# Kernel optimization log

Measured on AMD Instinct MI355X. Metric: run time of the kernel, lower is better.

Reference implementation:

```python
import jax, jax.numpy as jnp
import numpy as np

DIM = 1024
HEADS = 8
DIM_HEAD = 64
INNER = HEADS * DIM_HEAD  # 512


def setup_inputs() -> dict:
    key = jax.random.key(0)
    k1, k2, k3, k4 = jax.random.split(key, 4)
    x = jax.random.normal(k1, (4, 4096, DIM), dtype=jnp.float32)
    # torch nn.Linear weights: [out_features, in_features]
    w_qkv = jax.random.normal(k2, (INNER * 3, DIM), dtype=jnp.float32) * (DIM ** -0.5)
    w_out = jax.random.normal(k3, (DIM, INNER), dtype=jnp.float32) * (INNER ** -0.5)
    b_out = jax.random.normal(k4, (DIM,), dtype=jnp.float32) * 0.01
    return {"x": x, "w_qkv": w_qkv, "w_out": w_out, "b_out": b_out}


def reference(x, w_qkv, w_out, b_out):
    b, n, _ = x.shape
    h, dh = HEADS, DIM_HEAD
    qkv = x @ w_qkv.T  # [b, n, 3*inner]
    q, k, v = jnp.split(qkv, 3, axis=-1)
    # [b, n, inner] -> [b, h, n, dh]
    reshape = lambda t: t.reshape(b, n, h, dh).transpose(0, 2, 1, 3)
    q, k, v = reshape(q), reshape(k), reshape(v)
    k = jax.nn.softmax(k, axis=-1)
    context = jnp.einsum('bhnd,bhne->bhde', k, v)   # [b, h, dh, dh]
    out = jnp.einsum('bhnd,bhde->bhne', q, context)  # [b, h, n, dh]
    out = out.transpose(0, 2, 1, 3).reshape(b, n, h * dh)
    return out @ w_out.T + b_out
```

## Files before the change

### kernel.cpp

```cpp
#include <hip/hip_runtime.h>
#include <hip/hip_bf16.h>

using bf16 = __hip_bfloat16;
typedef __attribute__((ext_vector_type(8))) short short8;
typedef __attribute__((ext_vector_type(4))) float floatx4;

#define NB 4
#define NSEQ 4096
#define DIM 1024
#define INNER 512
#define TOK (NB * NSEQ)


__device__ inline unsigned short f2bf(float x) {
  union { bf16 h; unsigned short u; } c; c.h = __float2bfloat16(x); return c.u;
}
__device__ inline float bf2f(unsigned short u) {
  return __uint_as_float((unsigned)u << 16);
}

__device__ inline void stage8(const bf16* __restrict__ src, bf16* dst) {
  *(uint4*)dst = *(const uint4*)src;
}
__device__ inline void stage8(const float* __restrict__ src, bf16* dst) {
  const float4 a = ((const float4*)src)[0];
  const float4 b = ((const float4*)src)[1];
  union { uint4 u; bf16 h[8]; } p;
  p.h[0] = __float2bfloat16(a.x); p.h[1] = __float2bfloat16(a.y);
  p.h[2] = __float2bfloat16(a.z); p.h[3] = __float2bfloat16(a.w);
  p.h[4] = __float2bfloat16(b.x); p.h[5] = __float2bfloat16(b.y);
  p.h[6] = __float2bfloat16(b.z); p.h[7] = __float2bfloat16(b.w);
  *(uint4*)dst = p.u;
}

__global__ __launch_bounds__(256)
void convert_x(const float* __restrict__ x, bf16* __restrict__ xb) {
  const size_t i = (size_t)blockIdx.x * 256 + threadIdx.x;
  stage8(x + i * 8, xb + i * 8);
}

__global__ __launch_bounds__(256)
void copy16(const uint4* __restrict__ src, uint4* __restrict__ dst) {
  const size_t i = (size_t)blockIdx.x * 256 + threadIdx.x;
  dst[i] = src[i];
}

__global__ void zero_ctx(float* __restrict__ ctx) {
  ((float4*)ctx)[blockIdx.x * 256 + threadIdx.x] = make_float4(0.f, 0.f, 0.f, 0.f);
}

template <typename TA, typename TW, typename TO, bool BIAS>
__global__ __launch_bounds__(256, 4)
void gemm_bt(const TA* __restrict__ A, int lda,
             const TW* __restrict__ W, size_t wbatch,
             const float* __restrict__ bias,
             TO* __restrict__ C, int ldc, int K) {
  __shared__ __align__(16) bf16 As[128 * 72];
  __shared__ __align__(16) bf16 Bs[128 * 72];

  const int tid  = threadIdx.x;
  const int m0   = blockIdx.y * 128;
  const int n0   = blockIdx.x * 128;
  if (wbatch) W += (size_t)(blockIdx.y >> 5) * wbatch;

  const int wave = tid >> 6;
  const int lane = tid & 63;
  const int wr   = (wave >> 1) * 64;
  const int wc   = (wave & 1) * 64;
  const int quad = lane >> 4;
  const int r16  = lane & 15;

  floatx4 acc[4][4];
#pragma unroll
  for (int i = 0; i < 4; ++i)
#pragma unroll
    for (int j = 0; j < 4; ++j) acc[i][j] = (floatx4)0.0f;

  const int ksteps = K >> 6;
  for (int kt = 0; kt < ksteps; ++kt) {
    const int k0 = kt << 6;
#pragma unroll
    for (int l = 0; l < 4; ++l) {
      const int s   = l * 256 + tid;
      const int row = s >> 3, sub = s & 7;
      stage8(A + (size_t)(m0 + row) * lda + k0 + sub * 8, As + row * 72 + sub * 8);
      stage8(W + (size_t)(n0 + row) * K   + k0 + sub * 8, Bs + row * 72 + sub * 8);
    }
    __syncthreads();
#pragma unroll
    for (int kk = 0; kk < 64; kk += 32) {
      short8 af[4], bfg[4];
#pragma unroll
      for (int i = 0; i < 4; ++i)
        af[i] = *(const short8*)(As + (wr + i * 16 + r16) * 72 + kk + quad * 8);
#pragma unroll
      for (int j = 0; j < 4; ++j)
        bfg[j] = *(const short8*)(Bs + (wc + j * 16 + r16) * 72 + kk + quad * 8);
#pragma unroll
      for (int i = 0; i < 4; ++i)
#pragma unroll
        for (int j = 0; j < 4; ++j)
          acc[i][j] = __builtin_amdgcn_mfma_f32_16x16x32_bf16(af[i], bfg[j], acc[i][j], 0, 0, 0);
    }
    __syncthreads();
  }

#pragma unroll
  for (int j = 0; j < 4; ++j) {
    const int col = n0 + wc + j * 16 + r16;
    const float bv = BIAS ? bias[col] : 0.0f;
#pragma unroll
    for (int i = 0; i < 4; ++i) {
      const int rowb = m0 + wr + i * 16 + quad * 4;
#pragma unroll
      for (int r = 0; r < 4; ++r) {
        const float v = acc[i][j][r] + bv;
        if constexpr (sizeof(TO) == 2)
          C[(size_t)(rowb + r) * ldc + col] = __float2bfloat16(v);
        else
          C[(size_t)(rowb + r) * ldc + col] = v;
      }
    }
  }
}

__global__ __launch_bounds__(256)
void softmax_context(const unsigned short* __restrict__ kv, float* __restrict__ ctx) {
  __shared__ unsigned short skT[64 * 130];
  __shared__ unsigned short vT [64 * 130];

  const int tid   = threadIdx.x;
  const int wave  = tid >> 6;
  const int lane  = tid & 63;
  const int bh    = blockIdx.x >> 4;
  const int slice = blockIdx.x & 15;
  const int b     = bh >> 3, h = bh & 7;

  const int quad = lane >> 4;
  const int r16  = lane & 15;
  const int d0   = wave * 16;

  floatx4 acc[4];
#pragma unroll
  for (int j = 0; j < 4; ++j) acc[j] = (floatx4)0.0f;

  const int rgrp = tid >> 3;
  const int c    = tid & 7;

  for (int ch = 0; ch < 2; ++ch) {
#pragma unroll
    for (int p = 0; p < 4; ++p) {
      const int r = p * 32 + rgrp;
      const size_t rowbase =
          (size_t)(b * NSEQ + slice * 256 + ch * 128 + r) * 1024 + h * 64;
      const uint4 k8 = *(const uint4*)(kv + rowbase + c * 8);
      const uint4 v8 = *(const uint4*)(kv + rowbase + 512 + c * 8);
      const unsigned short* kb = (const unsigned short*)&k8;
      const unsigned short* vb = (const unsigned short*)&v8;

      float kf[8];
#pragma unroll
      for (int j = 0; j < 8; ++j) kf[j] = bf2f(kb[j]);
      float mx = kf[0];
#pragma unroll
      for (int j = 1; j < 8; ++j) mx = fmaxf(mx, kf[j]);
      mx = fmaxf(mx, __shfl_xor(mx, 1, 64));
      mx = fmaxf(mx, __shfl_xor(mx, 2, 64));
      mx = fmaxf(mx, __shfl_xor(mx, 4, 64));
      float e[8]; float s = 0.0f;
#pragma unroll
      for (int j = 0; j < 8; ++j) { e[j] = __expf(kf[j] - mx); s += e[j]; }
      s += __shfl_xor(s, 1, 64);
      s += __shfl_xor(s, 2, 64);
      s += __shfl_xor(s, 4, 64);
      const float inv = 1.0f / s;
#pragma unroll
      for (int j = 0; j < 8; ++j) {
        const int d = c * 8 + j;
        skT[d * 130 + r] = f2bf(e[j] * inv);
        vT [d * 130 + r] = vb[j];
      }
    }
    __syncthreads();

#pragma unroll
    for (int kk = 0; kk < 4; ++kk) {
      const int kof = kk * 32 + quad * 8;
      union { short8 v; unsigned u[4]; } afr;
      {
        const unsigned* q = (const unsigned*)(skT + (d0 + r16) * 130 + kof);
        afr.u[0] = q[0]; afr.u[1] = q[1]; afr.u[2] = q[2]; afr.u[3] = q[3];
      }
#pragma unroll
      for (int j = 0; j < 4; ++j) {
        union { short8 v; unsigned u[4]; } bfr;
        const unsigned* q = (const unsigned*)(vT + (j * 16 + r16) * 130 + kof);
        bfr.u[0] = q[0]; bfr.u[1] = q[1]; bfr.u[2] = q[2]; bfr.u[3] = q[3];
        acc[j] = __builtin_amdgcn_mfma_f32_16x16x32_bf16(afr.v, bfr.v, acc[j], 0, 0, 0);
      }
    }
    __syncthreads();
  }

  float* cg = ctx + (size_t)bh * 4096;
#pragma unroll
  for (int j = 0; j < 4; ++j) {
    const int e = j * 16 + r16;
#pragma unroll
    for (int r = 0; r < 4; ++r) {
      const int d = d0 + quad * 4 + r;
      atomicAdd(cg + d * 64 + e, acc[j][r]);
    }
  }
}

__global__ __launch_bounds__(256)
void transpose_wq(const float* __restrict__ wq, bf16* __restrict__ wqT) {
  __shared__ unsigned short t[64 * 68];
  const int tid = threadIdx.x;
  const int c0  = blockIdx.x * 64;
  const int r0  = blockIdx.y * 64;

#pragma unroll
  for (int l = 0; l < 4; ++l) {
    const int s = l * 256 + tid;
    const int row = s >> 4, col4 = s & 15;
    const float4 v = *(const float4*)(wq + (size_t)(r0 + row) * 1024 + c0 + col4 * 4);
    t[row * 68 + col4 * 4 + 0] = f2bf(v.x);
    t[row * 68 + col4 * 4 + 1] = f2bf(v.y);
    t[row * 68 + col4 * 4 + 2] = f2bf(v.z);
    t[row * 68 + col4 * 4 + 3] = f2bf(v.w);
  }
  __syncthreads();
#pragma unroll
  for (int l = 0; l < 2; ++l) {
    const int s = l * 256 + tid;
    const int cc = s >> 3, g = s & 7;
    union { uint4 u; unsigned short h[8]; } o;
#pragma unroll
    for (int u = 0; u < 8; ++u) o.h[u] = t[(g * 8 + u) * 68 + cc];
    *(uint4*)((unsigned short*)wqT + (size_t)(c0 + cc) * 512 + r0 + g * 8) = o.u;
  }
}

__global__ __launch_bounds__(256)
void build_m2(const float* __restrict__ w_out, const float* __restrict__ ctx,
              bf16* __restrict__ M2) {
  __shared__ unsigned short wo_s[128 * 68];
  __shared__ __align__(16) float ctx_s[4096];

  const int tid = threadIdx.x;
  const int bh  = blockIdx.y;
  const int b   = bh >> 3, h = bh & 7;
  const int o0  = blockIdx.x * 128;

#pragma unroll
  for (int l = 0; l < 8; ++l) {
    const int s = l * 256 + tid;
    const int row = s >> 4, col4 = s & 15;
    const float4 v = *(const float4*)(w_out + (size_t)(o0 + row) * 512 + h * 64 + col4 * 4);
    wo_s[row * 68 + col4 * 4 + 0] = f2bf(v.x);
    wo_s[row * 68 + col4 * 4 + 1] = f2bf(v.y);
    wo_s[row * 68 + col4 * 4 + 2] = f2bf(v.z);
    wo_s[row * 68 + col4 * 4 + 3] = f2bf(v.w);
  }
  const float4* cg = (const float4*)(ctx + (size_t)bh * 4096);
#pragma unroll
  for (int l = 0; l < 4; ++l) ((float4*)ctx_s)[l * 256 + tid] = cg[l * 256 + tid];
  __syncthreads();

  const int o_loc = tid & 127;
  const int dbase = (tid >> 7) * 32;
  float acc[32];
#pragma unroll
  for (int d = 0; d < 32; ++d) acc[d] = 0.0f;

  for (int e = 0; e < 64; ++e) {
    const float wf = bf2f(wo_s[o_loc * 68 + e]);
#pragma unroll
    for (int d = 0; d < 32; ++d)
      acc[d] += wf * ctx_s[(dbase + d) * 64 + e];
  }

  union { uint4 u[4]; unsigned short h[32]; } o;
#pragma unroll
  for (int d = 0; d < 32; ++d) o.h[d] = f2bf(acc[d]);
  unsigned short* dst = (unsigned short*)M2 + (size_t)(b * 1024 + o0 + o_loc) * 512 + h * 64 + dbase;
#pragma unroll
  for (int i = 0; i < 4; ++i) ((uint4*)dst)[i] = o.u[i];
}

extern "C" void kernel_launch(void* const* d_in, const int* in_sizes, int n_in,
                              void* d_out, int out_size, void* d_ws, size_t ws_size,
                              hipStream_t stream) {
  const float* x     = (const float*)d_in[0];
  const float* w_qkv = (const float*)d_in[1];
  const float* w_out = (const float*)d_in[2];
  const float* b_out = (const float*)d_in[3];
  float* out = (float*)d_out;

  char* xbuf = (char*)d_in[0];
  char* wbuf = (char*)d_in[1];

  bf16*  xb  = (bf16*)d_out;
  bf16*  kv  = (bf16*)xbuf;
  bf16*  M2  = (bf16*)(xbuf + (size_t)33554432);
  bf16*  W2  = (bf16*)(xbuf + (size_t)37748736);
  bf16*  xb2 = (bf16*)xbuf;
  bf16*  wqT = (bf16*)(wbuf + 2097152);
  float* ctx = (float*)(wbuf + 3145728);

  convert_x<<<8192, 256, 0, stream>>>(x, xb);

  gemm_bt<bf16, float, bf16, false><<<dim3(8, TOK / 128), 256, 0, stream>>>(
      xb, DIM, w_qkv + (size_t)INNER * DIM, 0, nullptr, kv, 1024, DIM);

  zero_ctx<<<128, 256, 0, stream>>>(ctx);
  transpose_wq<<<dim3(16, 8), 256, 0, stream>>>(w_qkv, wqT);

  softmax_context<<<512, 256, 0, stream>>>((const unsigned short*)kv, ctx);

  build_m2<<<dim3(8, 32), 256, 0, stream>>>(w_out, ctx, M2);

  gemm_bt<bf16, bf16, bf16, false><<<dim3(8, 32), 256, 0, stream>>>(
      M2, 512, wqT, 0, nullptr, W2, 1024, 512);

  copy16<<<8192, 256, 0, stream>>>((const uint4*)xb, (uint4*)xb2);

  gemm_bt<bf16, bf16, float, true><<<dim3(8, TOK / 128), 256, 0, stream>>>(
      xb2, DIM, W2, (size_t)1048576, b_out, out, DIM, DIM);
}
```

Measured before the change: 274.3 us.

## Stage GEMM tiles via direct global-to-LDS loads and split final GEMM

```diff
diff --git a/kernel.cpp b/kernel.cpp
--- a/kernel.cpp
+++ b/kernel.cpp
@@ -18,11 +18,7 @@
 __device__ inline float bf2f(unsigned short u) {
   return __uint_as_float((unsigned)u << 16);
 }
-
-__device__ inline void stage8(const bf16* __restrict__ src, bf16* dst) {
-  *(uint4*)dst = *(const uint4*)src;
-}
-__device__ inline void stage8(const float* __restrict__ src, bf16* dst) {
+__device__ inline void cvt8(const float* __restrict__ src, bf16* dst) {
   const float4 a = ((const float4*)src)[0];
   const float4 b = ((const float4*)src)[1];
   union { uint4 u; bf16 h[8]; } p;
@@ -33,10 +29,16 @@
   *(uint4*)dst = p.u;
 }
 
+__device__ inline void gload_lds16(const bf16* g, bf16* ldsbase) {
+  __builtin_amdgcn_global_load_lds(
+      (const __attribute__((address_space(1))) void*)g,
+      (__attribute__((address_space(3))) void*)ldsbase, 16, 0, 0);
+}
+
 __global__ __launch_bounds__(256)
 void convert_x(const float* __restrict__ x, bf16* __restrict__ xb) {
   const size_t i = (size_t)blockIdx.x * 256 + threadIdx.x;
-  stage8(x + i * 8, xb + i * 8);
+  cvt8(x + i * 8, xb + i * 8);
 }
 
 __global__ __launch_bounds__(256)
@@ -49,19 +51,22 @@
   ((float4*)ctx)[blockIdx.x * 256 + threadIdx.x] = make_float4(0.f, 0.f, 0.f, 0.f);
 }
 
-template <typename TA, typename TW, typename TO, bool BIAS>
+template <typename TO, bool BIAS>
 __global__ __launch_bounds__(256, 4)
-void gemm_bt(const TA* __restrict__ A, int lda,
-             const TW* __restrict__ W, size_t wbatch,
+void gemm_bt(const bf16* __restrict__ A, int lda,
+             const bf16* __restrict__ W, size_t wbatch, int mTiles,
              const float* __restrict__ bias,
              TO* __restrict__ C, int ldc, int K) {
-  __shared__ __align__(16) bf16 As[128 * 72];
-  __shared__ __align__(16) bf16 Bs[128 * 72];
-
-  const int tid  = threadIdx.x;
-  const int m0   = blockIdx.y * 128;
-  const int n0   = blockIdx.x * 128;
-  if (wbatch) W += (size_t)(blockIdx.y >> 5) * wbatch;
+  __shared__ __align__(16) bf16 As[128 * 64];
+  __shared__ __align__(16) bf16 Bs[128 * 64];
+
+  const int tid    = threadIdx.x;
+  const int p      = blockIdx.x;
+  const int m_tile = p % mTiles;
+  const int n_tile = p / mTiles;
+  const int m0     = m_tile * 128;
+  const int n0     = n_tile * 128;
+  if (wbatch) W += (size_t)(m_tile >> 5) * wbatch;
 
   const int wave = tid >> 6;
   const int lane = tid & 63;
@@ -69,6 +74,8 @@
   const int wc   = (wave & 1) * 64;
   const int quad = lane >> 4;
   const int r16  = lane & 15;
+  const int lrow = lane >> 3;
+  const int lcol = lane & 7;
 
   floatx4 acc[4][4];
 #pragma unroll
@@ -80,11 +87,11 @@
   for (int kt = 0; kt < ksteps; ++kt) {
     const int k0 = kt << 6;
 #pragma unroll
-    for (int l = 0; l < 4; ++l) {
-      const int s   = l * 256 + tid;
-      const int row = s >> 3, sub = s & 7;
-      stage8(A + (size_t)(m0 + row) * lda + k0 + sub * 8, As + row * 72 + sub * 8);
-      stage8(W + (size_t)(n0 + row) * K   + k0 + sub * 8, Bs + row * 72 + sub * 8);
+    for (int t = 0; t < 4; ++t) {
+      const int s   = wave * 4 + t;
+      const int row = s * 8 + lrow;
+      gload_lds16(A + (size_t)(m0 + row) * lda + k0 + lcol * 8, As + s * 512);
+      gload_lds16(W + (size_t)(n0 + row) * K   + k0 + lcol * 8, Bs + s * 512);
     }
     __syncthreads();
 #pragma unroll
@@ -92,10 +99,10 @@
       short8 af[4], bfg[4];
 #pragma unroll
       for (int i = 0; i < 4; ++i)
-        af[i] = *(const short8*)(As + (wr + i * 16 + r16) * 72 + kk + quad * 8);
+        af[i] = *(const short8*)(As + (wr + i * 16 + r16) * 64 + kk + quad * 8);
 #pragma unroll
       for (int j = 0; j < 4; ++j)
-        bfg[j] = *(const short8*)(Bs + (wc + j * 16 + r16) * 72 + kk + quad * 8);
+        bfg[j] = *(const short8*)(Bs + (wc + j * 16 + r16) * 64 + kk + quad * 8);
 #pragma unroll
       for (int i = 0; i < 4; ++i)
 #pragma unroll
@@ -302,18 +309,20 @@
   char* xbuf = (char*)d_in[0];
   char* wbuf = (char*)d_in[1];
 
-  bf16*  xb  = (bf16*)d_out;
-  bf16*  kv  = (bf16*)xbuf;
-  bf16*  M2  = (bf16*)(xbuf + (size_t)33554432);
-  bf16*  W2  = (bf16*)(xbuf + (size_t)37748736);
-  bf16*  xb2 = (bf16*)xbuf;
-  bf16*  wqT = (bf16*)(wbuf + 2097152);
-  float* ctx = (float*)(wbuf + 3145728);
+  bf16*  xb   = (bf16*)d_out;
+  bf16*  kv   = (bf16*)xbuf;
+  bf16*  M2   = (bf16*)(xbuf + (size_t)33554432);
+  bf16*  W2   = (bf16*)(xbuf + (size_t)37748736);
+  bf16*  wkvb = (bf16*)(xbuf + (size_t)50331648);
+  bf16*  xblo = (bf16*)xbuf;
+  bf16*  wqT  = (bf16*)(wbuf + 2097152);
+  float* ctx  = (float*)(wbuf + 3145728);
 
   convert_x<<<8192, 256, 0, stream>>>(x, xb);
-
-  gemm_bt<bf16, float, bf16, false><<<dim3(8, TOK / 128), 256, 0, stream>>>(
-      xb, DIM, w_qkv + (size_t)INNER * DIM, 0, nullptr, kv, 1024, DIM);
+  convert_x<<<512, 256, 0, stream>>>(w_qkv + (size_t)INNER * DIM, wkvb);
+
+  gemm_bt<bf16, false><<<1024, 256, 0, stream>>>(
+      xb, DIM, wkvb, 0, 128, nullptr, kv, 1024, DIM);
 
   zero_ctx<<<128, 256, 0, stream>>>(ctx);
   transpose_wq<<<dim3(16, 8), 256, 0, stream>>>(w_qkv, wqT);
@@ -322,11 +331,16 @@
 
   build_m2<<<dim3(8, 32), 256, 0, stream>>>(w_out, ctx, M2);
 
-  gemm_bt<bf16, bf16, bf16, false><<<dim3(8, 32), 256, 0, stream>>>(
-      M2, 512, wqT, 0, nullptr, W2, 1024, 512);
-
-  copy16<<<8192, 256, 0, stream>>>((const uint4*)xb, (uint4*)xb2);
-
-  gemm_bt<bf16, bf16, float, true><<<dim3(8, TOK / 128), 256, 0, stream>>>(
-      xb2, DIM, W2, (size_t)1048576, b_out, out, DIM, DIM);
-}
+  gemm_bt<bf16, false><<<256, 256, 0, stream>>>(
+      M2, 512, wqT, 0, 32, nullptr, W2, 1024, 512);
+
+  gemm_bt<float, true><<<512, 256, 0, stream>>>(
+      xb + (size_t)8192 * DIM, DIM, W2 + (size_t)2 * 1048576, (size_t)1048576, 64,
+      b_out, out + (size_t)8192 * DIM, DIM, DIM);
+
+  copy16<<<4096, 256, 0, stream>>>((const uint4*)xb, (uint4*)xblo);
+
+  gemm_bt<float, true><<<512, 256, 0, stream>>>(
+      xblo, DIM, W2, (size_t)1048576, 64,
+      b_out, out, DIM, DIM);
+}
```

Result: no change. 270.6 us (-1.3%).
